# Kernel tuning notes

Hardware: AMD Instinct MI355X
Metric: run time of the kernel (lower is better)

## Reference

```python
import jax, jax.numpy as jnp
import numpy as np

B, N, F, K = 512, 512, 512, 10
D = F // 2

def setup_inputs() -> dict:
    key = jax.random.key(0)
    k1, k2, k3 = jax.random.split(key, 3)
    ins_emb = jax.random.normal(k1, (B, N, F), dtype=jnp.float32)
    attn = jax.random.uniform(k2, (B, N, 1), dtype=jnp.float32)
    # xavier_uniform for a (D, D) linear weight
    limit = float(np.sqrt(6.0 / (D + D)))
    W = jax.random.uniform(k3, (D, D), dtype=jnp.float32, minval=-limit, maxval=limit)
    return {"ins_emb": ins_emb, "attn": attn, "W": W}

def reference(ins_emb, attn, W):
    d = ins_emb.shape[-1] // 2
    drug = ins_emb[:, :, :d]          # [B, N, d]
    dis = ins_emb[:, :, d:]           # [B, N, d]
    # torch Linear: drug @ W^T, then per-instance dot with dis -> scalar
    proj = jnp.einsum('bnd,ed->bne', drug, W)          # [B, N, d]
    pred = jnp.sum(proj * dis, axis=-1, keepdims=True) # [B, N, 1]
    attn_pred = attn * pred                            # [B, N, 1]
    topk_vals, _ = jax.lax.top_k(attn_pred[:, :, 0], K)  # [B, K]
    return jnp.mean(topk_vals, axis=1, keepdims=True)    # [B, 1]
```

## Files before the change

### kernel.cpp

```cpp
#include <hip/hip_runtime.h>
#include <hip/hip_bf16.h>
#include <cstdint>

#define BB 512
#define NN 512
#define FF 512
#define DD 256
#define KTOP 10
#define BN (BB*NN)
#define BM 64
#define NTILES (BN/BM)
#define GRID 256
#define TPB (NTILES/GRID)
#define LDAP 264

typedef __attribute__((ext_vector_type(8))) short bf16x8;
typedef __attribute__((ext_vector_type(4))) short s16x4;
typedef __attribute__((ext_vector_type(4))) float f32x4;

__device__ __forceinline__ ushort f2bf(float x){
  union { __hip_bfloat16 h; ushort u; } cv;
  cv.h = __float2bfloat16(x);
  return cv.u;
}
__device__ __forceinline__ float bf2f(ushort b){
  return __uint_as_float(((uint32_t)b) << 16);
}

__global__ void wconv(const float* __restrict__ W, ushort* __restrict__ Wbf){
  int i = (blockIdx.x*256 + threadIdx.x)*4;
  float4 v = *reinterpret_cast<const float4*>(W + i);
  s16x4 o;
  o[0] = (short)f2bf(v.x); o[1] = (short)f2bf(v.y);
  o[2] = (short)f2bf(v.z); o[3] = (short)f2bf(v.w);
  *reinterpret_cast<s16x4*>(Wbf + i) = o;
}

__global__ __launch_bounds__(512, 2)
void score_kernel(const float* __restrict__ emb, const float* __restrict__ attn,
                  const ushort* __restrict__ Wbf, float* __restrict__ scores){
  __shared__ ushort Abuf[2][BM*LDAP];
  __shared__ ushort Sbuf[2][BM*LDAP];
  __shared__ float red[8][BM];

  const int tid  = threadIdx.x;
  const int w    = tid >> 6;
  const int lane = tid & 63;
  const int g    = lane >> 4;
  const int c    = lane & 15;
  const int s    = w & 3;
  const int h    = w >> 2;

  bf16x8 Wf[4][4];
#pragma unroll
  for (int eb = 0; eb < 4; ++eb)
#pragma unroll
    for (int kb = 0; kb < 4; ++kb){
      int e = s*64 + eb*16 + c;
      int k = h*128 + kb*32 + g*8;
      Wf[eb][kb] = *reinterpret_cast<const bf16x8*>(Wbf + e*DD + k);
    }

  const int ch   = tid & 63;
  const int rsub = tid >> 6;
  const int tile0 = blockIdx.x * TPB;

  float4 pf[16];

#define PF_LOAD(TILE) do {                                                    \
    const float* base_ = emb + (size_t)(TILE)*BM*FF;                          \
    _Pragma("unroll")                                                         \
    for (int it = 0; it < 8; ++it){                                           \
      const float* src_ = base_ + (it*8 + rsub)*FF + ch*8;                    \
      pf[it*2]   = *reinterpret_cast<const float4*>(src_);                    \
      pf[it*2+1] = *reinterpret_cast<const float4*>(src_ + 4);                \
    }                                                                         \
  } while(0)

#define LDS_WRITE(BUFI) do {                                                  \
    _Pragma("unroll")                                                         \
    for (int it = 0; it < 8; ++it){                                           \
      int row_ = it*8 + rsub;                                                 \
      float4 a_ = pf[it*2], b_ = pf[it*2+1];                                  \
      bf16x8 p_;                                                              \
      p_[0]=(short)f2bf(a_.x); p_[1]=(short)f2bf(a_.y);                       \
      p_[2]=(short)f2bf(a_.z); p_[3]=(short)f2bf(a_.w);                       \
      p_[4]=(short)f2bf(b_.x); p_[5]=(short)f2bf(b_.y);                       \
      p_[6]=(short)f2bf(b_.z); p_[7]=(short)f2bf(b_.w);                       \
      ushort* dst_ = (ch < 32) ? &Abuf[BUFI][row_*LDAP + ch*8]                \
                               : &Sbuf[BUFI][row_*LDAP + (ch-32)*8];          \
      *reinterpret_cast<bf16x8*>(dst_) = p_;                                  \
    }                                                                         \
  } while(0)

  PF_LOAD(tile0);
  LDS_WRITE(0);
  __syncthreads();

  int cur = 0;
  for (int t = 0; t < TPB; ++t){
    const int tile = tile0 + t;
    if (t + 1 < TPB) PF_LOAD(tile + 1);

#pragma unroll
    for (int mb = 0; mb < 4; ++mb){
      const int m0 = mb*16;
      bf16x8 af[4];
#pragma unroll
      for (int kb = 0; kb < 4; ++kb)
        af[kb] = *reinterpret_cast<const bf16x8*>(
                     &Abuf[cur][(m0 + c)*LDAP + h*128 + kb*32 + g*8]);

      float rs0=0.f, rs1=0.f, rs2=0.f, rs3=0.f;
#pragma unroll
      for (int eb = 0; eb < 4; ++eb){
        f32x4 acc = {0.f, 0.f, 0.f, 0.f};
#pragma unroll
        for (int kb = 0; kb < 4; ++kb)
          acc = __builtin_amdgcn_mfma_f32_16x16x32_bf16(af[kb], Wf[eb][kb], acc, 0, 0, 0);
        const int e_loc = s*64 + eb*16 + c;
        rs0 += acc[0] * bf2f(Sbuf[cur][(m0 + g*4 + 0)*LDAP + e_loc]);
        rs1 += acc[1] * bf2f(Sbuf[cur][(m0 + g*4 + 1)*LDAP + e_loc]);
        rs2 += acc[2] * bf2f(Sbuf[cur][(m0 + g*4 + 2)*LDAP + e_loc]);
        rs3 += acc[3] * bf2f(Sbuf[cur][(m0 + g*4 + 3)*LDAP + e_loc]);
      }
      rs0 += __shfl_xor(rs0,1); rs0 += __shfl_xor(rs0,2); rs0 += __shfl_xor(rs0,4); rs0 += __shfl_xor(rs0,8);
      rs1 += __shfl_xor(rs1,1); rs1 += __shfl_xor(rs1,2); rs1 += __shfl_xor(rs1,4); rs1 += __shfl_xor(rs1,8);
      rs2 += __shfl_xor(rs2,1); rs2 += __shfl_xor(rs2,2); rs2 += __shfl_xor(rs2,4); rs2 += __shfl_xor(rs2,8);
      rs3 += __shfl_xor(rs3,1); rs3 += __shfl_xor(rs3,2); rs3 += __shfl_xor(rs3,4); rs3 += __shfl_xor(rs3,8);
      if (c == 0){
        red[w][m0 + g*4 + 0] = rs0;
        red[w][m0 + g*4 + 1] = rs1;
        red[w][m0 + g*4 + 2] = rs2;
        red[w][m0 + g*4 + 3] = rs3;
      }
    }
    __syncthreads();
    if (tid < BM){
      int row = tile*BM + tid;
      scores[row] = attn[row] * (red[0][tid] + red[1][tid] + red[2][tid] + red[3][tid]
                               + red[4][tid] + red[5][tid] + red[6][tid] + red[7][tid]);
    }
    if (t + 1 < TPB) LDS_WRITE(cur ^ 1);
    __syncthreads();
    cur ^= 1;
  }
#undef PF_LOAD
#undef LDS_WRITE
}

__global__ void topk_kernel(const float* __restrict__ scores, float* __restrict__ out){
  const int b = blockIdx.x;
  const int lane = threadIdx.x;
  float v0,v1,v2,v3,v4,v5,v6,v7;
  const float* sc = scores + b*NN;
  v0=sc[lane]; v1=sc[64+lane]; v2=sc[128+lane]; v3=sc[192+lane];
  v4=sc[256+lane]; v5=sc[320+lane]; v6=sc[384+lane]; v7=sc[448+lane];
  float total = 0.f;
  for (int it = 0; it < KTOP; ++it){
    float m = v0; int mj = 0;
    if (v1>m){m=v1;mj=1;} if (v2>m){m=v2;mj=2;} if (v3>m){m=v3;mj=3;}
    if (v4>m){m=v4;mj=4;} if (v5>m){m=v5;mj=5;} if (v6>m){m=v6;mj=6;}
    if (v7>m){m=v7;mj=7;}
    float bm = m; int bl = lane;
#pragma unroll
    for (int off = 32; off; off >>= 1){
      float om = __shfl_xor(bm, off);
      int   ol = __shfl_xor(bl, off);
      if (om > bm || (om == bm && ol < bl)){ bm = om; bl = ol; }
    }
    total += bm;
    if (lane == bl){
      if (mj==0) v0=-3.0e38f; else if (mj==1) v1=-3.0e38f;
      else if (mj==2) v2=-3.0e38f; else if (mj==3) v3=-3.0e38f;
      else if (mj==4) v4=-3.0e38f; else if (mj==5) v5=-3.0e38f;
      else if (mj==6) v6=-3.0e38f; else v7=-3.0e38f;
    }
  }
  if (lane == 0) out[b] = total * (1.0f / KTOP);
}

extern "C" void kernel_launch(void* const* d_in, const int* in_sizes, int n_in,
                              void* d_out, int out_size, void* d_ws, size_t ws_size,
                              hipStream_t stream){
  const float* emb  = (const float*)d_in[0];
  const float* attn = (const float*)d_in[1];
  const float* W    = (const float*)d_in[2];
  float* out = (float*)d_out;

  ushort* Wbf    = (ushort*)d_ws;
  float*  scores = (float*)((char*)d_ws + DD*DD*sizeof(ushort));

  wconv<<<64, 256, 0, stream>>>(W, Wbf);
  score_kernel<<<GRID, 512, 0, stream>>>(emb, attn, Wbf, scores);
  topk_kernel<<<BB, 64, 0, stream>>>(scores, out);
}
```

Measured before the change: 130.2 us.

## Stream fp32 tiles directly into swizzled LDS with async global_load_lds

Replaces the register-staged prefetch, which loaded fp32 rows, converted them to bf16 and wrote them to padded LDS, with `__builtin_amdgcn_global_load_lds` copies of raw fp32 rows into an XOR-swizzled LDS double buffer. Conversion to bf16 now happens when the MFMA operands are read, and the disease-half values are read as fp32 straight from LDS. The tile shrinks to 32 rows so the fp32 buffers fit. The reduction scratch is double-buffered so each iteration needs only one barrier, and attn is preloaded into LDS. The aim is to cut VGPR staging and barrier stalls and keep more loads in flight on this bandwidth-bound kernel. The cost is about 128KB of LDS, which limits the kernel to one block per CU, and extra conversion work on the read side.

```diff
diff --git a/kernel.cpp b/kernel.cpp
--- a/kernel.cpp
+++ b/kernel.cpp
@@ -8,11 +8,10 @@
 #define DD 256
 #define KTOP 10
 #define BN (BB*NN)
-#define BM 64
+#define BM 32
 #define NTILES (BN/BM)
 #define GRID 256
 #define TPB (NTILES/GRID)
-#define LDAP 264
 
 typedef __attribute__((ext_vector_type(8))) short bf16x8;
 typedef __attribute__((ext_vector_type(4))) short s16x4;
@@ -23,9 +22,19 @@
   cv.h = __float2bfloat16(x);
   return cv.u;
 }
-__device__ __forceinline__ float bf2f(ushort b){
-  return __uint_as_float(((uint32_t)b) << 16);
-}
+
+__device__ __forceinline__ bf16x8 cvt8(f32x4 a, f32x4 b){
+  bf16x8 r;
+  r[0]=(short)f2bf(a[0]); r[1]=(short)f2bf(a[1]); r[2]=(short)f2bf(a[2]); r[3]=(short)f2bf(a[3]);
+  r[4]=(short)f2bf(b[0]); r[5]=(short)f2bf(b[1]); r[6]=(short)f2bf(b[2]); r[7]=(short)f2bf(b[3]);
+  return r;
+}
+
+#define GL2LDS(GSRC, LDST)                                                          \
+  __builtin_amdgcn_global_load_lds(                                                 \
+      (const __attribute__((address_space(1))) uint32_t*)(uintptr_t)(GSRC),         \
+      (__attribute__((address_space(3))) uint32_t*)(uint32_t)(uintptr_t)(LDST),     \
+      16, 0, 0)
 
 __global__ void wconv(const float* __restrict__ W, ushort* __restrict__ Wbf){
   int i = (blockIdx.x*256 + threadIdx.x)*4;
@@ -39,9 +48,9 @@
 __global__ __launch_bounds__(512, 2)
 void score_kernel(const float* __restrict__ emb, const float* __restrict__ attn,
                   const ushort* __restrict__ Wbf, float* __restrict__ scores){
-  __shared__ ushort Abuf[2][BM*LDAP];
-  __shared__ ushort Sbuf[2][BM*LDAP];
-  __shared__ float red[8][BM];
+  __shared__ float Lbuf[2][BM*FF];
+  __shared__ float red[2][8][BM];
+  __shared__ float attn_l[TPB*BM];
 
   const int tid  = threadIdx.x;
   const int w    = tid >> 6;
@@ -51,6 +60,9 @@
   const int s    = w & 3;
   const int h    = w >> 2;
 
+  attn_l[tid]       = attn[blockIdx.x*(TPB*BM) + tid];
+  attn_l[tid + 512] = attn[blockIdx.x*(TPB*BM) + 512 + tid];
+
   bf16x8 Wf[4][4];
 #pragma unroll
   for (int eb = 0; eb < 4; ++eb)
@@ -61,56 +73,43 @@
       Wf[eb][kb] = *reinterpret_cast<const bf16x8*>(Wbf + e*DD + k);
     }
 
-  const int ch   = tid & 63;
-  const int rsub = tid >> 6;
-  const int tile0 = blockIdx.x * TPB;
-
-  float4 pf[16];
-
-#define PF_LOAD(TILE) do {                                                    \
-    const float* base_ = emb + (size_t)(TILE)*BM*FF;                          \
-    _Pragma("unroll")                                                         \
-    for (int it = 0; it < 8; ++it){                                           \
-      const float* src_ = base_ + (it*8 + rsub)*FF + ch*8;                    \
-      pf[it*2]   = *reinterpret_cast<const float4*>(src_);                    \
-      pf[it*2+1] = *reinterpret_cast<const float4*>(src_ + 4);                \
-    }                                                                         \
-  } while(0)
-
-#define LDS_WRITE(BUFI) do {                                                  \
-    _Pragma("unroll")                                                         \
-    for (int it = 0; it < 8; ++it){                                           \
-      int row_ = it*8 + rsub;                                                 \
-      float4 a_ = pf[it*2], b_ = pf[it*2+1];                                  \
-      bf16x8 p_;                                                              \
-      p_[0]=(short)f2bf(a_.x); p_[1]=(short)f2bf(a_.y);                       \
-      p_[2]=(short)f2bf(a_.z); p_[3]=(short)f2bf(a_.w);                       \
-      p_[4]=(short)f2bf(b_.x); p_[5]=(short)f2bf(b_.y);                       \
-      p_[6]=(short)f2bf(b_.z); p_[7]=(short)f2bf(b_.w);                       \
-      ushort* dst_ = (ch < 32) ? &Abuf[BUFI][row_*LDAP + ch*8]                \
-                               : &Sbuf[BUFI][row_*LDAP + (ch-32)*8];          \
-      *reinterpret_cast<bf16x8*>(dst_) = p_;                                  \
-    }                                                                         \
-  } while(0)
-
-  PF_LOAD(tile0);
-  LDS_WRITE(0);
+  int offs[8];
+#pragma unroll
+  for (int i = 0; i < 8; ++i){
+    int idx = w*8 + i;
+    int r = idx >> 1, hf = idx & 1;
+    offs[i] = r*FF + hf*256 + ((lane ^ (r & 7)) << 2);
+  }
+  const float* tbase = emb + (size_t)blockIdx.x * TPB * (BM*FF);
+
+#pragma unroll
+  for (int i = 0; i < 8; ++i)
+    GL2LDS(tbase + offs[i], &Lbuf[0][(w*8 + i)*256]);
   __syncthreads();
 
   int cur = 0;
   for (int t = 0; t < TPB; ++t){
-    const int tile = tile0 + t;
-    if (t + 1 < TPB) PF_LOAD(tile + 1);
-
-#pragma unroll
-    for (int mb = 0; mb < 4; ++mb){
+    if (t + 1 < TPB){
+      const float* nb = tbase + (size_t)(t+1) * (BM*FF);
+#pragma unroll
+      for (int i = 0; i < 8; ++i)
+        GL2LDS(nb + offs[i], &Lbuf[cur ^ 1][(w*8 + i)*256]);
+    }
+
+    const f32x4* Lv = (const f32x4*)&Lbuf[cur][0];
+#pragma unroll
+    for (int mb = 0; mb < 2; ++mb){
       const int m0 = mb*16;
+      const int rb = (m0 + c)*128;
+      const int x  = c & 7;
       bf16x8 af[4];
 #pragma unroll
-      for (int kb = 0; kb < 4; ++kb)
-        af[kb] = *reinterpret_cast<const bf16x8*>(
-                     &Abuf[cur][(m0 + c)*LDAP + h*128 + kb*32 + g*8]);
-
+      for (int kb = 0; kb < 4; ++kb){
+        int ch0 = h*32 + kb*8 + g*2;
+        f32x4 q0 = Lv[rb + ((ch0    ) ^ x)];
+        f32x4 q1 = Lv[rb + ((ch0 + 1) ^ x)];
+        af[kb] = cvt8(q0, q1);
+      }
       float rs0=0.f, rs1=0.f, rs2=0.f, rs3=0.f;
 #pragma unroll
       for (int eb = 0; eb < 4; ++eb){
@@ -118,35 +117,41 @@
 #pragma unroll
         for (int kb = 0; kb < 4; ++kb)
           acc = __builtin_amdgcn_mfma_f32_16x16x32_bf16(af[kb], Wf[eb][kb], acc, 0, 0, 0);
-        const int e_loc = s*64 + eb*16 + c;
-        rs0 += acc[0] * bf2f(Sbuf[cur][(m0 + g*4 + 0)*LDAP + e_loc]);
-        rs1 += acc[1] * bf2f(Sbuf[cur][(m0 + g*4 + 1)*LDAP + e_loc]);
-        rs2 += acc[2] * bf2f(Sbuf[cur][(m0 + g*4 + 2)*LDAP + e_loc]);
-        rs3 += acc[3] * bf2f(Sbuf[cur][(m0 + g*4 + 3)*LDAP + e_loc]);
+        const int sb = 64 + s*16 + eb*4 + (c >> 2);
+        const int e3 = c & 3;
+#pragma unroll
+        for (int j = 0; j < 4; ++j){
+          const int row = m0 + g*4 + j;
+          const int fi  = row*FF + ((sb ^ (row & 7)) << 2) + e3;
+          float d = Lbuf[cur][fi];
+          if      (j == 0) rs0 += acc[0]*d;
+          else if (j == 1) rs1 += acc[1]*d;
+          else if (j == 2) rs2 += acc[2]*d;
+          else             rs3 += acc[3]*d;
+        }
       }
       rs0 += __shfl_xor(rs0,1); rs0 += __shfl_xor(rs0,2); rs0 += __shfl_xor(rs0,4); rs0 += __shfl_xor(rs0,8);
       rs1 += __shfl_xor(rs1,1); rs1 += __shfl_xor(rs1,2); rs1 += __shfl_xor(rs1,4); rs1 += __shfl_xor(rs1,8);
       rs2 += __shfl_xor(rs2,1); rs2 += __shfl_xor(rs2,2); rs2 += __shfl_xor(rs2,4); rs2 += __shfl_xor(rs2,8);
       rs3 += __shfl_xor(rs3,1); rs3 += __shfl_xor(rs3,2); rs3 += __shfl_xor(rs3,4); rs3 += __shfl_xor(rs3,8);
       if (c == 0){
-        red[w][m0 + g*4 + 0] = rs0;
-        red[w][m0 + g*4 + 1] = rs1;
-        red[w][m0 + g*4 + 2] = rs2;
-        red[w][m0 + g*4 + 3] = rs3;
+        red[cur][w][m0 + g*4 + 0] = rs0;
+        red[cur][w][m0 + g*4 + 1] = rs1;
+        red[cur][w][m0 + g*4 + 2] = rs2;
+        red[cur][w][m0 + g*4 + 3] = rs3;
       }
     }
+
     __syncthreads();
+
     if (tid < BM){
-      int row = tile*BM + tid;
-      scores[row] = attn[row] * (red[0][tid] + red[1][tid] + red[2][tid] + red[3][tid]
-                               + red[4][tid] + red[5][tid] + red[6][tid] + red[7][tid]);
-    }
-    if (t + 1 < TPB) LDS_WRITE(cur ^ 1);
-    __syncthreads();
+      float sum = red[cur][0][tid] + red[cur][1][tid] + red[cur][2][tid] + red[cur][3][tid]
+                + red[cur][4][tid] + red[cur][5][tid] + red[cur][6][tid] + red[cur][7][tid];
+      int row = (blockIdx.x*TPB + t)*BM + tid;
+      scores[row] = attn_l[t*BM + tid] * sum;
+    }
     cur ^= 1;
   }
-#undef PF_LOAD
-#undef LDS_WRITE
 }
 
 __global__ void topk_kernel(const float* __restrict__ scores, float* __restrict__ out){
```

Measured after the change: 110.0 us. 1.18x faster.
